# Optimization experiments

Hardware: AMD Instinct MI355X
Metric: run time of the kernel (lower is better)

## Reference

```python
import jax, jax.numpy as jnp
import numpy as np

# shift search range (matches init_kwargs)
MIN_SX, MAX_SX = -4, 4
MIN_SY, MAX_SY = -4, 4
B, C, H, W = 4, 3, 512, 512


def _shift(x, sx, sy):
    """torch.roll on dims (1,2) of a [C,H,W] tensor, zeroing wrapped rows/cols.

    Equivalent to AutomatedShiftFix.shift: positive sx zeros rows [:sx],
    negative sx zeros rows [sx:]; same for sy on the W axis.
    """
    h, w = x.shape[1], x.shape[2]
    shifted = jnp.roll(x, (sx, sy), axis=(1, 2))
    i = jnp.arange(h)[:, None]   # [H,1]
    j = jnp.arange(w)[None, :]   # [1,W]
    mask_h = jnp.where(sx >= 0, i >= sx, i < h + sx)
    mask_w = jnp.where(sy >= 0, j >= sy, j < w + sy)
    mask = (mask_h & mask_w).astype(x.dtype)  # [H,W]
    return shifted * mask[None]


def _all_shifts():
    sx = jnp.arange(MIN_SX, MAX_SX + 1)
    sy = jnp.arange(MIN_SY, MAX_SY + 1)
    # outer loop over shift_x, inner over shift_y -> 'ij' matches torch ordering
    return jnp.stack(jnp.meshgrid(sx, sy, indexing="ij"), axis=-1).reshape(-1, 2)  # [Ns,2]


def setup_inputs() -> dict:
    key = jax.random.key(0)
    k1, k2 = jax.random.split(key)
    x_ref = jax.random.normal(k1, (B, C, H, W), dtype=jnp.float32)
    x = jax.random.normal(k2, (B, C, H, W), dtype=jnp.float32)
    return {"x_ref": x_ref, "x": x}


def reference(x_ref, x):
    shifts = _all_shifts()  # [Ns,2] int32

    def sims_one(xr, xi):  # xr, xi: [C,H,W]
        # similarity for every candidate shift: sum over (C,H,W) of shifted*ref
        return jax.vmap(lambda s: jnp.sum(_shift(xi, s[0], s[1]) * xr))(shifts)  # [Ns]

    sims = jax.vmap(sims_one)(x_ref, x)          # [B, Ns]
    best = jnp.argmax(sims, axis=1)              # [B]
    best_shifts = shifts[best]                   # [B, 2]
    out = jax.vmap(lambda xi, s: _shift(xi, s[0], s[1]))(x, best_shifts)  # [B,C,H,W]
    return out, best_shifts
```

## Files before the change

### kernel.cpp

```cpp
#include <hip/hip_runtime.h>

#define BB 4
#define CC 3
#define HH 512
#define WW 512
#define NS 81
#define IMG (HH * WW)
#define CHW (CC * IMG)
#define STRIP 32
#define NSTRIP (HH / STRIP)
#define NBLK (BB * CC * NSTRIP * 9)


#define C4(v, i) ((i) == 0 ? (v).x : (i) == 1 ? (v).y : (i) == 2 ? (v).z : (v).w)

__global__ __launch_bounds__(256, 4) void k_sims(const float* __restrict__ xref,
                                                 const float* __restrict__ x,
                                                 double* __restrict__ sims) {
    int bid  = blockIdx.x;
    int sxi  = bid % 9;
    int tmp  = bid / 9;
    int strip = tmp % NSTRIP;
    int bc   = tmp / NSTRIP;
    int b    = bc / CC;
    const float* xp = x    + (size_t)bc * IMG;
    const float* rp = xref + (size_t)bc * IMG;
    int tid  = threadIdx.x;
    int lane = tid & 63;
    int wave = tid >> 6;
    int j0   = lane << 3;
    int sx   = sxi - 4;
    int ip0  = strip * STRIP + wave * 8;

    float acc[9];
#pragma unroll
    for (int s = 0; s < 9; ++s) acc[s] = 0.f;

#pragma unroll
    for (int rr = 0; rr < 8; ++rr) {
        int ip = ip0 + rr;
        int ii = ip + sx;
        if ((unsigned)ii >= HH) continue;

        const float* xrow = xp + ip * WW + j0;
        const float* rrow = rp + ii * WW + j0;
        float4 xa = *(const float4*)(xrow);
        float4 xb = *(const float4*)(xrow + 4);
        float4 ra = *(const float4*)(rrow);
        float4 rb = *(const float4*)(rrow + 4);

        float p0 = __shfl_up(rb.x, 1, 64);
        float p1 = __shfl_up(rb.y, 1, 64);
        float p2 = __shfl_up(rb.z, 1, 64);
        float p3 = __shfl_up(rb.w, 1, 64);
        if (lane == 0) { p0 = p1 = p2 = p3 = 0.f; }
        float n0 = __shfl_down(ra.x, 1, 64);
        float n1 = __shfl_down(ra.y, 1, 64);
        float n2 = __shfl_down(ra.z, 1, 64);
        float n3 = __shfl_down(ra.w, 1, 64);
        if (lane == 63) { n0 = n1 = n2 = n3 = 0.f; }

#define P4(i) ((i) == 0 ? p0 : (i) == 1 ? p1 : (i) == 2 ? p2 : p3)
#define N4(i) ((i) == 0 ? n0 : (i) == 1 ? n1 : (i) == 2 ? n2 : n3)
#pragma unroll
        for (int syi = 0; syi < 9; ++syi) {
#pragma unroll
            for (int k = 0; k < 8; ++k) {
                int i = k + syi;
                float wv = (i < 4)  ? P4(i)
                         : (i < 8)  ? C4(ra, i - 4)
                         : (i < 12) ? C4(rb, i - 8)
                         :            N4(i - 12);
                float xv = (k < 4) ? C4(xa, k) : C4(xb, k - 4);
                acc[syi] += xv * wv;
            }
        }
#undef P4
#undef N4
    }

    __shared__ float part[4][9];
#pragma unroll
    for (int s = 0; s < 9; ++s) {
        float v = acc[s];
        for (int off = 32; off; off >>= 1) v += __shfl_down(v, off, 64);
        if (lane == 0) part[wave][s] = v;
    }
    __syncthreads();
    if (tid < 9) {
        double tot = (double)part[0][tid] + (double)part[1][tid]
                   + (double)part[2][tid] + (double)part[3][tid];
        atomicAdd(&sims[b * NS + sxi * 9 + tid], tot);
    }
}

__global__ __launch_bounds__(256) void k_apply(const float* __restrict__ x,
                                               const double* __restrict__ sims,
                                               float* __restrict__ out,
                                               float* __restrict__ outTail) {
    int blk = blockIdx.x;
    int bc  = blk >> 8;
    int tid = threadIdx.x;
    int b   = bc / CC;

    __shared__ double vals[NS];
    __shared__ int bestIdx;
    if (tid < NS) vals[tid] = sims[b * NS + tid];
    __syncthreads();
    if (tid < 64) {
        double v = vals[tid];
        int    i = tid;
        if (tid < NS - 64) {
            double v2 = vals[tid + 64];
            if (v2 > v) { v = v2; i = tid + 64; }
        }
        for (int off = 32; off; off >>= 1) {
            double ov = __shfl_down(v, off, 64);
            int    oi = __shfl_down(i, off, 64);
            if (ov > v || (ov == v && oi < i)) { v = ov; i = oi; }
        }
        if (tid == 0) bestIdx = i;
    }
    __syncthreads();
    int bi = bestIdx;
    int sx = bi / 9 - 4;
    int sy = bi % 9 - 4;
    if (blk == ((b * CC) << 8) && tid == 0) {
        outTail[b * 2]     = (float)sx;
        outTail[b * 2 + 1] = (float)sy;
    }

    int row = ((blk & 255) << 1) + (tid >> 7);
    int j0  = (tid & 127) << 2;
    int is  = row - sx;
    float4 v = make_float4(0.f, 0.f, 0.f, 0.f);
    if ((unsigned)is < HH) {
        const float* src = x + (size_t)bc * IMG + is * WW;
        int js0 = j0 - sy;
        if (js0 >= 0 && js0 + 3 < WW) {
            v = *(const float4*)(src + js0);
        } else {
            float* vv = (float*)&v;
#pragma unroll
            for (int k = 0; k < 4; ++k) {
                int js = js0 + k;
                if ((unsigned)js < WW) vv[k] = src[js];
            }
        }
    }
    *(float4*)(out + (size_t)bc * IMG + row * WW + j0) = v;
}

extern "C" void kernel_launch(void* const* d_in, const int* in_sizes, int n_in,
                              void* d_out, int out_size, void* d_ws, size_t ws_size,
                              hipStream_t stream) {
    const float* xref = (const float*)d_in[0];
    const float* x    = (const float*)d_in[1];
    float* out = (float*)d_out;

    double* sims = (double*)d_ws;

    hipMemsetAsync(sims, 0, BB * NS * sizeof(double), stream);

    k_sims<<<NBLK, 256, 0, stream>>>(xref, x, sims);

    int applyBlocks = (BB * CC * HH) / 2;
    k_apply<<<applyBlocks, 256, 0, stream>>>(x, sims, out, out + (size_t)BB * CHW);
}
```

Before: 107.1 us.

## Replace atomics with per-block partials, add reduce kernel, load neighbors directly

Each sims block now writes its partial sums to a global buffer instead of doing double-precision atomicAdds, which also removes the memset. A small new reduction kernel sums the partials and takes the argmax once per batch, so the apply kernel no longer repeats the 81-way argmax in every block. The neighbor reference values used for the horizontal shifts are now loaded directly from memory instead of exchanged with cross-lane shuffles. In exchange the pipeline gains an extra kernel launch, and the neighbor data costs extra, mostly cache-hitting, loads.

Measured after the change: 111.5 us. +4.1%, slower.

```diff
diff --git a/kernel.cpp b/kernel.cpp
--- a/kernel.cpp
+++ b/kernel.cpp
@@ -11,18 +11,18 @@
 #define NSTRIP (HH / STRIP)
 #define NBLK (BB * CC * NSTRIP * 9)
 
+__device__ double g_part[NBLK][9];
+__device__ int    g_best[BB];
 
 #define C4(v, i) ((i) == 0 ? (v).x : (i) == 1 ? (v).y : (i) == 2 ? (v).z : (v).w)
 
 __global__ __launch_bounds__(256, 4) void k_sims(const float* __restrict__ xref,
-                                                 const float* __restrict__ x,
-                                                 double* __restrict__ sims) {
+                                                 const float* __restrict__ x) {
     int bid  = blockIdx.x;
     int sxi  = bid % 9;
     int tmp  = bid / 9;
     int strip = tmp % NSTRIP;
     int bc   = tmp / NSTRIP;
-    int b    = bc / CC;
     const float* xp = x    + (size_t)bc * IMG;
     const float* rp = xref + (size_t)bc * IMG;
     int tid  = threadIdx.x;
@@ -46,37 +46,29 @@
         const float* rrow = rp + ii * WW + j0;
         float4 xa = *(const float4*)(xrow);
         float4 xb = *(const float4*)(xrow + 4);
+
+        const float4* pp = (const float4*)(rrow + (lane == 0  ? 0 : -4));
+        const float4* np = (const float4*)(rrow + (lane == 63 ? 0 :  8));
+        float4 pv = *pp;
         float4 ra = *(const float4*)(rrow);
         float4 rb = *(const float4*)(rrow + 4);
+        float4 nv = *np;
+        if (lane == 0)  pv = make_float4(0.f, 0.f, 0.f, 0.f);
+        if (lane == 63) nv = make_float4(0.f, 0.f, 0.f, 0.f);
 
-        float p0 = __shfl_up(rb.x, 1, 64);
-        float p1 = __shfl_up(rb.y, 1, 64);
-        float p2 = __shfl_up(rb.z, 1, 64);
-        float p3 = __shfl_up(rb.w, 1, 64);
-        if (lane == 0) { p0 = p1 = p2 = p3 = 0.f; }
-        float n0 = __shfl_down(ra.x, 1, 64);
-        float n1 = __shfl_down(ra.y, 1, 64);
-        float n2 = __shfl_down(ra.z, 1, 64);
-        float n3 = __shfl_down(ra.w, 1, 64);
-        if (lane == 63) { n0 = n1 = n2 = n3 = 0.f; }
-
-#define P4(i) ((i) == 0 ? p0 : (i) == 1 ? p1 : (i) == 2 ? p2 : p3)
-#define N4(i) ((i) == 0 ? n0 : (i) == 1 ? n1 : (i) == 2 ? n2 : n3)
 #pragma unroll
         for (int syi = 0; syi < 9; ++syi) {
 #pragma unroll
             for (int k = 0; k < 8; ++k) {
                 int i = k + syi;
-                float wv = (i < 4)  ? P4(i)
+                float wv = (i < 4)  ? C4(pv, i)
                          : (i < 8)  ? C4(ra, i - 4)
                          : (i < 12) ? C4(rb, i - 8)
-                         :            N4(i - 12);
+                         :            C4(nv, i - 12);
                 float xv = (k < 4) ? C4(xa, k) : C4(xb, k - 4);
                 acc[syi] += xv * wv;
             }
         }
-#undef P4
-#undef N4
     }
 
     __shared__ float part[4][9];
@@ -88,47 +80,50 @@
     }
     __syncthreads();
     if (tid < 9) {
-        double tot = (double)part[0][tid] + (double)part[1][tid]
-                   + (double)part[2][tid] + (double)part[3][tid];
-        atomicAdd(&sims[b * NS + sxi * 9 + tid], tot);
+        g_part[bid][tid] = (double)part[0][tid] + (double)part[1][tid]
+                         + (double)part[2][tid] + (double)part[3][tid];
+    }
+}
+
+__global__ __launch_bounds__(128) void k_reduce(float* __restrict__ outTail) {
+    int b = blockIdx.x;
+    int t = threadIdx.x;
+    __shared__ double vals[NS];
+    if (t < NS) {
+        int sxi = t / 9;
+        int syi = t % 9;
+        double s = 0.0;
+#pragma unroll
+        for (int c = 0; c < CC; ++c)
+#pragma unroll
+            for (int st = 0; st < NSTRIP; ++st) {
+                int bid = ((b * CC + c) * NSTRIP + st) * 9 + sxi;
+                s += g_part[bid][syi];
+            }
+        vals[t] = s;
+    }
+    __syncthreads();
+    if (t == 0) {
+        int best = 0;
+        double bv = vals[0];
+        for (int i = 1; i < NS; ++i)
+            if (vals[i] > bv) { bv = vals[i]; best = i; }
+        g_best[b] = best;
+        outTail[b * 2]     = (float)(best / 9 - 4);
+        outTail[b * 2 + 1] = (float)(best % 9 - 4);
     }
 }
 
 __global__ __launch_bounds__(256) void k_apply(const float* __restrict__ x,
-                                               const double* __restrict__ sims,
-                                               float* __restrict__ out,
-                                               float* __restrict__ outTail) {
+                                               float* __restrict__ out) {
     int blk = blockIdx.x;
     int bc  = blk >> 8;
     int tid = threadIdx.x;
     int b   = bc / CC;
 
-    __shared__ double vals[NS];
-    __shared__ int bestIdx;
-    if (tid < NS) vals[tid] = sims[b * NS + tid];
-    __syncthreads();
-    if (tid < 64) {
-        double v = vals[tid];
-        int    i = tid;
-        if (tid < NS - 64) {
-            double v2 = vals[tid + 64];
-            if (v2 > v) { v = v2; i = tid + 64; }
-        }
-        for (int off = 32; off; off >>= 1) {
-            double ov = __shfl_down(v, off, 64);
-            int    oi = __shfl_down(i, off, 64);
-            if (ov > v || (ov == v && oi < i)) { v = ov; i = oi; }
-        }
-        if (tid == 0) bestIdx = i;
-    }
-    __syncthreads();
-    int bi = bestIdx;
+    int bi = g_best[b];
     int sx = bi / 9 - 4;
     int sy = bi % 9 - 4;
-    if (blk == ((b * CC) << 8) && tid == 0) {
-        outTail[b * 2]     = (float)sx;
-        outTail[b * 2 + 1] = (float)sy;
-    }
 
     int row = ((blk & 255) << 1) + (tid >> 7);
     int j0  = (tid & 127) << 2;
@@ -157,13 +152,11 @@
     const float* xref = (const float*)d_in[0];
     const float* x    = (const float*)d_in[1];
     float* out = (float*)d_out;
+    (void)d_ws; (void)ws_size;
 
-    double* sims = (double*)d_ws;
-
-    hipMemsetAsync(sims, 0, BB * NS * sizeof(double), stream);
-
-    k_sims<<<NBLK, 256, 0, stream>>>(xref, x, sims);
+    k_sims<<<NBLK, 256, 0, stream>>>(xref, x);
+    k_reduce<<<BB, 128, 0, stream>>>(out + (size_t)BB * CHW);
 
     int applyBlocks = (BB * CC * HH) / 2;
-    k_apply<<<applyBlocks, 256, 0, stream>>>(x, sims, out, out + (size_t)BB * CHW);
+    k_apply<<<applyBlocks, 256, 0, stream>>>(x, out);
 }
```
